# Optimization experiments

Measured on AMD Instinct MI355X. Metric: run time of the kernel, lower is better.

Reference implementation:

```python
import jax, jax.numpy as jnp
import numpy as np


def conv2d(x, w, b, pad):
    # NCHW / OIHW conv, stride 1
    y = jax.lax.conv_general_dilated(x, w, (1, 1), [(pad, pad), (pad, pad)],
                                     dimension_numbers=('NCHW', 'OIHW', 'NCHW'))
    return y + b[None, :, None, None]


def deform_conv2d(x, offset, modulator, w_reg, b_reg):
    # Faithful reimplementation of torchvision.ops.deform_conv2d (stride=1,
    # pad=K//2, dilation=1, 1 offset group), offset layout [B, 2*K*K, H, W]
    # with (dy, dx) pairs per kernel tap.
    B, C, H, W = x.shape
    K = w_reg.shape[-1]
    KK = K * K
    pad = K // 2
    off = offset.reshape(B, KK, 2, H, W)
    ks_y = (jnp.arange(KK) // K - pad).astype(x.dtype)
    ks_x = (jnp.arange(KK) % K - pad).astype(x.dtype)
    hh = jnp.arange(H, dtype=x.dtype)
    ww = jnp.arange(W, dtype=x.dtype)
    # sampling coords per (batch, kernel tap, out_y, out_x)
    py = hh[None, None, :, None] + ks_y[None, :, None, None] + off[:, :, 0]
    px = ww[None, None, None, :] + ks_x[None, :, None, None] + off[:, :, 1]
    y0 = jnp.floor(py)
    x0 = jnp.floor(px)
    ly = py - y0
    lx = px - x0
    y0i = y0.astype(jnp.int32)
    x0i = x0.astype(jnp.int32)
    x_flat = x.reshape(B, C, H * W)

    def gather(yi, xi, wgt):
        valid = (yi >= 0) & (yi < H) & (xi >= 0) & (xi < W)
        idx = (jnp.clip(yi, 0, H - 1) * W + jnp.clip(xi, 0, W - 1)).reshape(B, KK, H * W)
        v = jnp.take_along_axis(x_flat[:, :, None, :], idx[:, None], axis=3)  # [B,C,KK,HW]
        w = (wgt * valid.astype(x.dtype)).reshape(B, 1, KK, H * W)
        return v * w

    v = (gather(y0i, x0i, (1 - ly) * (1 - lx))
         + gather(y0i, x0i + 1, (1 - ly) * lx)
         + gather(y0i + 1, x0i, ly * (1 - lx))
         + gather(y0i + 1, x0i + 1, ly * lx))
    v = v * modulator.reshape(B, 1, KK, H * W)
    out = jnp.einsum('bckn,ock->bon', v, w_reg.reshape(w_reg.shape[0], C, KK))
    return out.reshape(B, -1, H, W) + b_reg[None, :, None, None]


def setup_inputs() -> dict:
    key = jax.random.key(0)
    ks = jax.random.split(key, 14)
    B, C, H, W = 8, 256, 64, 64
    K = 3
    Cr = C // 4  # SE ratio=4
    x = jax.random.normal(ks[0], (B, C, H, W), jnp.float32)
    # small offset-conv weights keep sampled offsets modest (torchvision inits these to 0)
    w_off = jax.random.normal(ks[1], (2 * K * K, C, K, K), jnp.float32) * 0.01
    b_off = jax.random.normal(ks[2], (2 * K * K,), jnp.float32) * 0.01
    w_mod = jax.random.normal(ks[3], (K * K, C, K, K), jnp.float32) * 0.01
    b_mod = jax.random.normal(ks[4], (K * K,), jnp.float32) * 0.01
    w_reg = jax.random.normal(ks[5], (C, C, K, K), jnp.float32) * (1.0 / np.sqrt(C * K * K))
    b_reg = jax.random.normal(ks[6], (C,), jnp.float32) * 0.01
    w_se1 = jax.random.normal(ks[7], (Cr, C), jnp.float32) * (1.0 / np.sqrt(C))
    b_se1 = jnp.zeros((Cr,), jnp.float32)
    w_se2 = jax.random.normal(ks[8], (C, Cr), jnp.float32) * (1.0 / np.sqrt(Cr))
    b_se2 = jnp.zeros((C,), jnp.float32)
    w_mask = jax.random.normal(ks[9], (C, C, 1, 1), jnp.float32) * (1.0 / np.sqrt(C))
    b_mask = jnp.zeros((C,), jnp.float32)
    return {"x": x, "w_off": w_off, "b_off": b_off, "w_mod": w_mod, "b_mod": b_mod,
            "w_reg": w_reg, "b_reg": b_reg, "w_se1": w_se1, "b_se1": b_se1,
            "w_se2": w_se2, "b_se2": b_se2, "w_mask": w_mask, "b_mask": b_mask}


def reference(x, w_off, b_off, w_mod, b_mod, w_reg, b_reg,
              w_se1, b_se1, w_se2, b_se2, w_mask, b_mask):
    # DeformableConv2d
    offset = conv2d(x, w_off, b_off, pad=1)
    modulator = 2.0 * jax.nn.sigmoid(conv2d(x, w_mod, b_mod, pad=1))
    f = deform_conv2d(x, offset, modulator, w_reg, b_reg)
    # SEBlock('avg', ch, ratio=4)
    s = jnp.mean(f, axis=(2, 3))                       # [B, C]
    s = jax.nn.relu(s @ w_se1.T + b_se1)               # [B, C/4]
    s = jax.nn.sigmoid(s @ w_se2.T + b_se2)            # [B, C]
    f = f * s[:, :, None, None]
    # mask = Hardsigmoid(Conv1x1(x))
    m = conv2d(x, w_mask, b_mask, pad=0)
    m = jnp.clip(m / 6.0 + 0.5, 0.0, 1.0)
    return f * m + x
```

## Files before the change

### kernel.cpp

```cpp
#include <hip/hip_runtime.h>
#include <math.h>

#define HWSZ 4096
#define C_ 256
#define B_ 8

#define M_WS      0
#define XB_WS     4194304
#define WT2_WS    8388608
#define SMEAN_WS  8753152
#define SSCALE_WS 8755200

typedef __attribute__((ext_vector_type(8))) short short8;
typedef __attribute__((ext_vector_type(4))) float f32x4;

__device__ __forceinline__ uint bfr(float a) {
  uint u = __float_as_uint(a);
  return (u + 0x7fffu + ((u >> 16) & 1u)) >> 16;
}
__device__ __forceinline__ uint pk2(float a, float b) { return bfr(a) | (bfr(b) << 16); }
__device__ __forceinline__ float bff(ushort u) { return __uint_as_float((uint)u << 16); }
__device__ __forceinline__ float lo16(uint u) { return __uint_as_float(u << 16); }
__device__ __forceinline__ float hi16(uint u) { return __uint_as_float(u & 0xffff0000u); }

__global__ __launch_bounds__(256) void k0_weights(
    const float* __restrict__ w_reg, const float* __restrict__ w_mask,
    const float* __restrict__ w_off, const float* __restrict__ w_mod,
    float* __restrict__ ws) {
  int i = blockIdx.x * 256 + threadIdx.x;
  const int nwt = 10 * 65536;
  const int total = nwt + 9 * 32 * 256;
  if (i >= total) {
    int z = i - total;
    if (z < 2048) ws[SMEAN_WS + z] = 0.f;
    return;
  }
  float v;
  if (i < 9 * 65536) {
    int kk = i >> 16, o = (i >> 8) & 255, c = i & 255;
    v = w_reg[(o * C_ + c) * 9 + kk];
  } else if (i < nwt) {
    v = w_mask[i - 9 * 65536];
  } else {
    int e = i - nwt;
    int s = e >> 13, r = e & 8191;
    int o2 = r >> 8, c = r & 255;
    if (o2 < 18)      v = w_off[(o2 * C_ + c) * 9 + s];
    else if (o2 < 27) v = w_mod[((o2 - 18) * C_ + c) * 9 + s];
    else              v = 0.f;
  }
  ((ushort*)(ws + WT2_WS))[i] = (ushort)bfr(v);
}

__global__ __launch_bounds__(256) void k0b_nhwc(const float* __restrict__ x,
                                                float* __restrict__ ws) {
  __shared__ float tile[64][65];
  int b = blockIdx.x >> 6, hw0 = (blockIdx.x & 63) << 6;
  int t = threadIdx.x;
  uint* xb = (uint*)(ws + XB_WS) + ((size_t)b << 19);
  int rr = t >> 6, cc = t & 63;
  int e = t & 7, hwp = t >> 3;
  for (int cg = 0; cg < 4; cg++) {
    __syncthreads();
    const float* xp = x + ((size_t)(b * 256 + cg * 64 + rr)) * HWSZ + hw0 + cc;
    #pragma unroll
    for (int r0 = 0; r0 < 64; r0 += 4)
      tile[r0 + rr][cc] = xp[(size_t)r0 * HWSZ];
    __syncthreads();
    #pragma unroll
    for (int h2 = 0; h2 < 2; h2++) {
      int hw_l = h2 * 32 + hwp;
      int c2 = e * 8;
      uint4 val;
      val.x = pk2(tile[c2][hw_l], tile[c2 + 1][hw_l]);
      val.y = pk2(tile[c2 + 2][hw_l], tile[c2 + 3][hw_l]);
      val.z = pk2(tile[c2 + 4][hw_l], tile[c2 + 5][hw_l]);
      val.w = pk2(tile[c2 + 6][hw_l], tile[c2 + 7][hw_l]);
      *(uint4*)&xb[(size_t)(hw0 + hw_l) * 128 + cg * 32 + e * 4] = val;
    }
  }
}

__global__ __launch_bounds__(512, 4) void k2_fused(
    const float* __restrict__ b_off, const float* __restrict__ b_mod,
    const float* __restrict__ b_reg, const float* __restrict__ b_mask,
    float* __restrict__ ws, float* __restrict__ out) {
  __shared__ uint vbraw[2][66 * 128];
  __shared__ float omrf[9 * 64 * 4];

  int bl = ((blockIdx.x & 7) << 6) | (blockIdx.x >> 3);
  int b = bl >> 6, h = bl & 63;
  int t = threadIdx.x;
  int lane = t & 63, w = t >> 6;
  const int hwid = t >> 5;
  const int cl = lane & 31;
  const ushort* xb2 = (const ushort*)(ws + XB_WS) + ((size_t)b << 20);
  const ushort* wt2 = (const ushort*)(ws + WT2_WS);
  const ushort* wom = wt2 + 10 * 65536;
  const int fr = lane & 15, fq = lane >> 4;

  auto widxP = [&](int pcol) -> uint {
    return (uint)pcol * 128u + (((uint)cl * 4u) ^ ((uint)(pcol & 7) << 2));
  };
  auto stageRow = [&](int row, int buf) {
    bool rv = ((unsigned)row < 64u);
    #pragma unroll
    for (int p = 0; p < 4; p++) {
      int pcol = p * 16 + hwid;
      int col = pcol - 1;
      uint4 v = make_uint4(0, 0, 0, 0);
      if (rv && ((unsigned)col < 64u))
        v = *(const uint4*)(xb2 + ((size_t)(row * 64 + col)) * 256 + cl * 8);
      *(uint4*)&vbraw[buf][widxP(pcol)] = v;
    }
    if (hwid < 2) {
      int pcol = 64 + hwid;
      int col = pcol - 1;
      uint4 v = make_uint4(0, 0, 0, 0);
      if (rv && col < 64)
        v = *(const uint4*)(xb2 + ((size_t)(row * 64 + col)) * 256 + cl * 8);
      *(uint4*)&vbraw[buf][widxP(pcol)] = v;
    }
  };
  auto makeRecs = [&](int kk, int nl, float* wg, int* ix) {
    const float4 rec = *(const float4*)&omrf[kk * 256 + nl * 4];
    float dy = rec.x, dx = rec.y, md = rec.z;
    float py = (float)(h + kk / 3 - 1) + dy;
    float px = (float)(nl + kk % 3 - 1) + dx;
    float fy = floorf(py), fx = floorf(px);
    float ly = py - fy, lx = px - fx;
    int y0 = (int)fy, x0 = (int)fx;
    int y1 = y0 + 1, x1 = x0 + 1;
    float vy0 = ((unsigned)y0 < 64u) ? 1.f : 0.f;
    float vy1 = ((unsigned)y1 < 64u) ? 1.f : 0.f;
    float vx0 = ((unsigned)x0 < 64u) ? 1.f : 0.f;
    float vx1 = ((unsigned)x1 < 64u) ? 1.f : 0.f;
    int cy0 = min(max(y0, 0), 63), cy1 = min(max(y1, 0), 63);
    int cx0 = min(max(x0, 0), 63), cx1 = min(max(x1, 0), 63);
    ix[0] = cy0 * 64 + cx0; wg[0] = (1.f - ly) * (1.f - lx) * md * vy0 * vx0;
    ix[1] = cy0 * 64 + cx1; wg[1] = (1.f - ly) * lx * md * vy0 * vx1;
    ix[2] = cy1 * 64 + cx0; wg[2] = ly * (1.f - lx) * md * vy1 * vx0;
    ix[3] = cy1 * 64 + cx1; wg[3] = ly * lx * md * vy1 * vx1;
  };
  auto gatherTap = [&](int kk, int buf) {
    #pragma unroll
    for (int p = 0; p < 4; p++) {
      int n = p * 16 + hwid;
      float wg[4]; int ix[4];
      makeRecs(kk, n, wg, ix);
      float a0 = 0.f, a1 = 0.f, a2 = 0.f, a3 = 0.f, a4 = 0.f, a5 = 0.f, a6 = 0.f, a7 = 0.f;
      #pragma unroll
      for (int cr = 0; cr < 4; cr++) {
        uint4 dd = *(const uint4*)(xb2 + (size_t)ix[cr] * 256 + cl * 8);
        float wv = wg[cr];
        a0 = fmaf(wv, lo16(dd.x), a0); a1 = fmaf(wv, hi16(dd.x), a1);
        a2 = fmaf(wv, lo16(dd.y), a2); a3 = fmaf(wv, hi16(dd.y), a3);
        a4 = fmaf(wv, lo16(dd.z), a4); a5 = fmaf(wv, hi16(dd.z), a5);
        a6 = fmaf(wv, lo16(dd.w), a6); a7 = fmaf(wv, hi16(dd.w), a7);
      }
      *(uint4*)&vbraw[buf][widxP(n)] =
          make_uint4(pk2(a0, a1), pk2(a2, a3), pk2(a4, a5), pk2(a6, a7));
    }
  };

  f32x4 aom = (f32x4)0.f;
  const int m0 = w >> 2, nt0 = w & 3;
  const int o0 = w << 5;
  f32x4 acc[2][4];
  #pragma unroll
  for (int mt = 0; mt < 2; mt++)
    #pragma unroll
    for (int nt = 0; nt < 4; nt++) acc[mt][nt] = (f32x4)0.f;
  ushort* mws = (ushort*)(ws + M_WS);
  float* sme = ws + SMEAN_WS + b * 256;

  stageRow(h - 1, 0);
  __syncthreads();
  for (int e = 0; e < 3; e++) {
    const int buf = (e == 1) ? 1 : 0;
    {
      const int bnA = nt0 * 16 + fr;
      #pragma unroll
      for (int s3 = 0; s3 < 3; s3++) {
        int s = e * 3 + s3;
        const ushort* wp = wom + (size_t)s * 8192;
        int pcol = bnA + s3;
        for (int ks = 0; ks < 8; ks++) {
          short8 af = *(const short8*)(wp + (m0 * 16 + fr) * 256 + ks * 32 + fq * 8);
          uint idx = (uint)pcol * 128u + (((uint)(ks * 16 + fq * 4)) ^ ((uint)(pcol & 7) << 2));
          short8 bf = *(const short8*)&vbraw[buf][idx];
          aom = __builtin_amdgcn_mfma_f32_16x16x32_bf16(af, bf, aom, 0, 0, 0);
        }
      }
    }
    if (e == 1) {
      const ushort* wt9 = wt2 + (size_t)9 * 65536;
      __builtin_amdgcn_s_setprio(1);
      for (int ks = 0; ks < 8; ks++) {
        short8 af0 = *(const short8*)(wt9 + (o0 + fr) * 256 + ks * 32 + fq * 8);
        short8 af1 = *(const short8*)(wt9 + (o0 + 16 + fr) * 256 + ks * 32 + fq * 8);
        #pragma unroll
        for (int nt = 0; nt < 4; nt++) {
          int pcol = nt * 16 + fr + 1;
          uint idx = (uint)pcol * 128u + (((uint)(ks * 16 + fq * 4)) ^ ((uint)(pcol & 7) << 2));
          short8 bf = *(const short8*)&vbraw[1][idx];
          acc[0][nt] = __builtin_amdgcn_mfma_f32_16x16x32_bf16(af0, bf, acc[0][nt], 0, 0, 0);
          acc[1][nt] = __builtin_amdgcn_mfma_f32_16x16x32_bf16(af1, bf, acc[1][nt], 0, 0, 0);
        }
      }
      __builtin_amdgcn_s_setprio(0);
    }
    if (e == 0)      stageRow(h, 1);
    else if (e == 1) stageRow(h + 1, 0);
    else {
      #pragma unroll
      for (int mt = 0; mt < 2; mt++)
        #pragma unroll
        for (int r = 0; r < 4; r++) {
          int o = o0 + mt * 16 + fq * 4 + r;
          float bm = b_mask[o];
          ushort* mp = mws + (size_t)(b * C_ + o) * HWSZ + h * 64;
          #pragma unroll
          for (int nt = 0; nt < 4; nt++) {
            float mv = fminf(fmaxf((acc[mt][nt][r] + bm) * (1.f / 6.f) + 0.5f, 0.f), 1.f);
            mp[nt * 16 + fr] = (ushort)bfr(mv);
            acc[mt][nt][r] = 0.f;
          }
        }
      #pragma unroll
      for (int r = 0; r < 4; r++) {
        int o = m0 * 16 + fq * 4 + r;
        int nn = nt0 * 16 + fr;
        if (o < 18) {
          omrf[(o >> 1) * 256 + nn * 4 + (o & 1)] = aom[r] + b_off[o];
        } else if (o < 27) {
          float v = aom[r] + b_mod[o - 18];
          omrf[(o - 18) * 256 + nn * 4 + 2] = 2.f / (1.f + expf(-v));
        }
      }
    }
    __syncthreads();
  }

  gatherTap(0, 1);
  __syncthreads();
  for (int kk = 0; kk < 9; kk++) {
    const int cur = (kk & 1) ^ 1;
    const ushort* wtap = wt2 + (size_t)kk * 65536;
    __builtin_amdgcn_s_setprio(1);
    for (int ks = 0; ks < 8; ks++) {
      short8 af0 = *(const short8*)(wtap + (o0 + fr) * 256 + ks * 32 + fq * 8);
      short8 af1 = *(const short8*)(wtap + (o0 + 16 + fr) * 256 + ks * 32 + fq * 8);
      #pragma unroll
      for (int nt = 0; nt < 4; nt++) {
        int bn = nt * 16 + fr;
        uint idx = (uint)bn * 128u + (((uint)(ks * 16 + fq * 4)) ^ ((uint)(bn & 7) << 2));
        short8 bf = *(const short8*)&vbraw[cur][idx];
        acc[0][nt] = __builtin_amdgcn_mfma_f32_16x16x32_bf16(af0, bf, acc[0][nt], 0, 0, 0);
        acc[1][nt] = __builtin_amdgcn_mfma_f32_16x16x32_bf16(af1, bf, acc[1][nt], 0, 0, 0);
      }
    }
    __builtin_amdgcn_s_setprio(0);
    if (kk < 8) {
      gatherTap(kk + 1, cur ^ 1);
      __syncthreads();
    }
  }

  #pragma unroll
  for (int mt = 0; mt < 2; mt++)
    #pragma unroll
    for (int r = 0; r < 4; r++) {
      int o = o0 + mt * 16 + fq * 4 + r;
      float bo = b_reg[o];
      float* op = out + (size_t)(b * C_ + o) * HWSZ + h * 64;
      float so = 0.f;
      #pragma unroll
      for (int nt = 0; nt < 4; nt++) {
        float fv = acc[mt][nt][r] + bo;
        op[nt * 16 + fr] = fv;
        so += fv;
      }
      so += __shfl_xor(so, 1);
      so += __shfl_xor(so, 2);
      so += __shfl_xor(so, 4);
      so += __shfl_xor(so, 8);
      if (fr == 0) atomicAdd(&sme[o], so);
    }
}

__global__ __launch_bounds__(256) void k4_se(
    const float* __restrict__ w_se1, const float* __restrict__ b_se1,
    const float* __restrict__ w_se2, const float* __restrict__ b_se2,
    float* __restrict__ ws) {
  __shared__ float sm[256];
  __shared__ float s1[64];
  int b = blockIdx.x;
  int t = threadIdx.x;
  sm[t] = ws[SMEAN_WS + b * 256 + t] * (1.f / HWSZ);
  __syncthreads();
  if (t < 64) {
    float a = b_se1[t];
    for (int c = 0; c < 256; c++) a += sm[c] * w_se1[t * 256 + c];
    s1[t] = fmaxf(a, 0.f);
  }
  __syncthreads();
  {
    float a = b_se2[t];
    for (int cr = 0; cr < 64; cr++) a += s1[cr] * w_se2[t * 64 + cr];
    ws[SSCALE_WS + b * 256 + t] = 1.f / (1.f + expf(-a));
  }
}

__global__ __launch_bounds__(256) void k5_final(const float* __restrict__ x,
                                                const float* __restrict__ ws,
                                                float* __restrict__ out) {
  const ushort* mws = (const ushort*)(ws + M_WS);
  int i4 = blockIdx.x * 256 + threadIdx.x;
  const int total = B_ * C_ * HWSZ / 4;
  for (; i4 < total; i4 += gridDim.x * 256) {
    int i = i4 * 4;
    int bc = i >> 12;
    float s = ws[SSCALE_WS + bc];
    float4 f = *(const float4*)&out[i];
    uint2 mu = *(const uint2*)&mws[i];
    float4 xv = *(const float4*)&x[i];
    float4 r;
    r.x = f.x * s * bff((ushort)(mu.x & 0xffffu)) + xv.x;
    r.y = f.y * s * bff((ushort)(mu.x >> 16)) + xv.y;
    r.z = f.z * s * bff((ushort)(mu.y & 0xffffu)) + xv.z;
    r.w = f.w * s * bff((ushort)(mu.y >> 16)) + xv.w;
    *(float4*)&out[i] = r;
  }
}

extern "C" void kernel_launch(void* const* d_in, const int* in_sizes, int n_in,
                              void* d_out, int out_size, void* d_ws, size_t ws_size,
                              hipStream_t stream) {
  const float* x      = (const float*)d_in[0];
  const float* w_off  = (const float*)d_in[1];
  const float* b_off  = (const float*)d_in[2];
  const float* w_mod  = (const float*)d_in[3];
  const float* b_mod  = (const float*)d_in[4];
  const float* w_reg  = (const float*)d_in[5];
  const float* b_reg  = (const float*)d_in[6];
  const float* w_se1  = (const float*)d_in[7];
  const float* b_se1  = (const float*)d_in[8];
  const float* w_se2  = (const float*)d_in[9];
  const float* b_se2  = (const float*)d_in[10];
  const float* w_mask = (const float*)d_in[11];
  const float* b_mask = (const float*)d_in[12];
  float* out = (float*)d_out;
  float* ws  = (float*)d_ws;

  k0_weights<<<dim3(2856), dim3(256), 0, stream>>>(w_reg, w_mask, w_off, w_mod, ws);
  k0b_nhwc<<<dim3(512), dim3(256), 0, stream>>>(x, ws);
  k2_fused<<<dim3(512), dim3(512), 0, stream>>>(b_off, b_mod, b_reg, b_mask, ws, out);
  k4_se<<<dim3(8), dim3(256), 0, stream>>>(w_se1, b_se1, w_se2, b_se2, ws);
  k5_final<<<dim3(2048), dim3(256), 0, stream>>>(x, ws, out);
}
```

Measured before the change: 194.8 us.

## Process two output rows per block to share staged input rows

The fused deformable-conv kernel now has 1024-thread blocks, each covering two adjacent output rows, with 256 blocks instead of 512. Each half of the block runs the offset/modulator and mask convolutions for its own row. The halves share the four staged input rows, where two single-row blocks staged six. The gather and tap GEMM loop then fill and consume a 128-column LDS buffer. This cuts redundant input staging and repeated weight fetches, but the larger LDS footprint allows only one block per CU and lengthens the per-block critical path.

```diff
diff --git a/kernel.cpp b/kernel.cpp
--- a/kernel.cpp
+++ b/kernel.cpp
@@ -81,51 +81,43 @@
   }
 }
 
-__global__ __launch_bounds__(512, 4) void k2_fused(
+__global__ __launch_bounds__(1024, 4) void k2_fused(
     const float* __restrict__ b_off, const float* __restrict__ b_mod,
     const float* __restrict__ b_reg, const float* __restrict__ b_mask,
     float* __restrict__ ws, float* __restrict__ out) {
-  __shared__ uint vbraw[2][66 * 128];
-  __shared__ float omrf[9 * 64 * 4];
-
-  int bl = ((blockIdx.x & 7) << 6) | (blockIdx.x >> 3);
-  int b = bl >> 6, h = bl & 63;
+  __shared__ uint vb[2][128 * 128];
+  __shared__ float omrf[2 * 9 * 64 * 4];
+
+  int bl = ((blockIdx.x & 7) << 5) | (blockIdx.x >> 3);
+  int b = bl >> 5, h0 = (bl & 31) << 1;
   int t = threadIdx.x;
   int lane = t & 63, w = t >> 6;
-  const int hwid = t >> 5;
+  const int hw = t >> 5;
   const int cl = lane & 31;
   const ushort* xb2 = (const ushort*)(ws + XB_WS) + ((size_t)b << 20);
   const ushort* wt2 = (const ushort*)(ws + WT2_WS);
   const ushort* wom = wt2 + 10 * 65536;
   const int fr = lane & 15, fq = lane >> 4;
-
-  auto widxP = [&](int pcol) -> uint {
-    return (uint)pcol * 128u + (((uint)cl * 4u) ^ ((uint)(pcol & 7) << 2));
+  const int rowhalf = w >> 3;
+  const int wv8 = w & 7;
+
+  auto widx = [&](int P) -> uint {
+    return (uint)P * 128u + (((uint)cl * 4u) ^ ((uint)(P & 7) << 2));
   };
   auto stageRow = [&](int row, int buf) {
     bool rv = ((unsigned)row < 64u);
-    #pragma unroll
-    for (int p = 0; p < 4; p++) {
-      int pcol = p * 16 + hwid;
-      int col = pcol - 1;
+    for (int pc = hw; pc < 66; pc += 32) {
+      int col = pc - 1;
       uint4 v = make_uint4(0, 0, 0, 0);
       if (rv && ((unsigned)col < 64u))
         v = *(const uint4*)(xb2 + ((size_t)(row * 64 + col)) * 256 + cl * 8);
-      *(uint4*)&vbraw[buf][widxP(pcol)] = v;
-    }
-    if (hwid < 2) {
-      int pcol = 64 + hwid;
-      int col = pcol - 1;
-      uint4 v = make_uint4(0, 0, 0, 0);
-      if (rv && col < 64)
-        v = *(const uint4*)(xb2 + ((size_t)(row * 64 + col)) * 256 + cl * 8);
-      *(uint4*)&vbraw[buf][widxP(pcol)] = v;
+      *(uint4*)&vb[buf][widx(pc)] = v;
     }
   };
-  auto makeRecs = [&](int kk, int nl, float* wg, int* ix) {
-    const float4 rec = *(const float4*)&omrf[kk * 256 + nl * 4];
+  auto makeRecs = [&](int rloc, int kk, int nl, float* wg, int* ix) {
+    const float4 rec = *(const float4*)&omrf[((rloc * 9 + kk) * 64 + nl) * 4];
     float dy = rec.x, dx = rec.y, md = rec.z;
-    float py = (float)(h + kk / 3 - 1) + dy;
+    float py = (float)(h0 + rloc + kk / 3 - 1) + dy;
     float px = (float)(nl + kk % 3 - 1) + dx;
     float fy = floorf(py), fx = floorf(px);
     float ly = py - fy, lx = px - fx;
@@ -145,9 +137,9 @@
   auto gatherTap = [&](int kk, int buf) {
     #pragma unroll
     for (int p = 0; p < 4; p++) {
-      int n = p * 16 + hwid;
+      int P = p * 32 + hw;
       float wg[4]; int ix[4];
-      makeRecs(kk, n, wg, ix);
+      makeRecs(P >> 6, kk, P & 63, wg, ix);
       float a0 = 0.f, a1 = 0.f, a2 = 0.f, a3 = 0.f, a4 = 0.f, a5 = 0.f, a6 = 0.f, a7 = 0.f;
       #pragma unroll
       for (int cr = 0; cr < 4; cr++) {
@@ -158,14 +150,15 @@
         a4 = fmaf(wv, lo16(dd.z), a4); a5 = fmaf(wv, hi16(dd.z), a5);
         a6 = fmaf(wv, lo16(dd.w), a6); a7 = fmaf(wv, hi16(dd.w), a7);
       }
-      *(uint4*)&vbraw[buf][widxP(n)] =
+      *(uint4*)&vb[buf][widx(P)] =
           make_uint4(pk2(a0, a1), pk2(a2, a3), pk2(a4, a5), pk2(a6, a7));
     }
   };
 
   f32x4 aom = (f32x4)0.f;
-  const int m0 = w >> 2, nt0 = w & 3;
-  const int o0 = w << 5;
+  const int m0 = wv8 >> 2, nt0 = wv8 & 3;
+  const int o0 = wv8 << 5;
+  const int hme = h0 + rowhalf;
   f32x4 acc[2][4];
   #pragma unroll
   for (int mt = 0; mt < 2; mt++)
@@ -174,26 +167,28 @@
   ushort* mws = (ushort*)(ws + M_WS);
   float* sme = ws + SMEAN_WS + b * 256;
 
-  stageRow(h - 1, 0);
-  __syncthreads();
-  for (int e = 0; e < 3; e++) {
-    const int buf = (e == 1) ? 1 : 0;
-    {
+  stageRow(h0 - 1, 0);
+  __syncthreads();
+  for (int e = 0; e < 4; e++) {
+    const int buf = e & 1;
+    const int g = (rowhalf == 0) ? e : e - 1;
+    if (g >= 0 && g < 3) {
       const int bnA = nt0 * 16 + fr;
       #pragma unroll
       for (int s3 = 0; s3 < 3; s3++) {
-        int s = e * 3 + s3;
+        int s = g * 3 + s3;
         const ushort* wp = wom + (size_t)s * 8192;
         int pcol = bnA + s3;
+        uint idxb = (uint)pcol * 128u;
+        uint xr = (uint)(pcol & 7) << 2;
         for (int ks = 0; ks < 8; ks++) {
           short8 af = *(const short8*)(wp + (m0 * 16 + fr) * 256 + ks * 32 + fq * 8);
-          uint idx = (uint)pcol * 128u + (((uint)(ks * 16 + fq * 4)) ^ ((uint)(pcol & 7) << 2));
-          short8 bf = *(const short8*)&vbraw[buf][idx];
+          short8 bf = *(const short8*)&vb[buf][idxb + (((uint)(ks * 16 + fq * 4)) ^ xr)];
           aom = __builtin_amdgcn_mfma_f32_16x16x32_bf16(af, bf, aom, 0, 0, 0);
         }
       }
     }
-    if (e == 1) {
+    if ((rowhalf == 0 && e == 1) || (rowhalf == 1 && e == 2)) {
       const ushort* wt9 = wt2 + (size_t)9 * 65536;
       __builtin_amdgcn_s_setprio(1);
       for (int ks = 0; ks < 8; ks++) {
@@ -203,23 +198,22 @@
         for (int nt = 0; nt < 4; nt++) {
           int pcol = nt * 16 + fr + 1;
           uint idx = (uint)pcol * 128u + (((uint)(ks * 16 + fq * 4)) ^ ((uint)(pcol & 7) << 2));
-          short8 bf = *(const short8*)&vbraw[1][idx];
+          short8 bf = *(const short8*)&vb[buf][idx];
           acc[0][nt] = __builtin_amdgcn_mfma_f32_16x16x32_bf16(af0, bf, acc[0][nt], 0, 0, 0);
           acc[1][nt] = __builtin_amdgcn_mfma_f32_16x16x32_bf16(af1, bf, acc[1][nt], 0, 0, 0);
         }
       }
       __builtin_amdgcn_s_setprio(0);
     }
-    if (e == 0)      stageRow(h, 1);
-    else if (e == 1) stageRow(h + 1, 0);
-    else {
+    if (e < 3) stageRow(h0 + e, (e + 1) & 1);
+    if (e == 3 && rowhalf == 0) {
       #pragma unroll
       for (int mt = 0; mt < 2; mt++)
         #pragma unroll
         for (int r = 0; r < 4; r++) {
           int o = o0 + mt * 16 + fq * 4 + r;
           float bm = b_mask[o];
-          ushort* mp = mws + (size_t)(b * C_ + o) * HWSZ + h * 64;
+          ushort* mp = mws + (size_t)(b * C_ + o) * HWSZ + hme * 64;
           #pragma unroll
           for (int nt = 0; nt < 4; nt++) {
             float mv = fminf(fmaxf((acc[mt][nt][r] + bm) * (1.f / 6.f) + 0.5f, 0.f), 1.f);
@@ -232,20 +226,49 @@
         int o = m0 * 16 + fq * 4 + r;
         int nn = nt0 * 16 + fr;
         if (o < 18) {
-          omrf[(o >> 1) * 256 + nn * 4 + (o & 1)] = aom[r] + b_off[o];
+          omrf[((0 * 9 + (o >> 1)) * 64 + nn) * 4 + (o & 1)] = aom[r] + b_off[o];
         } else if (o < 27) {
           float v = aom[r] + b_mod[o - 18];
-          omrf[(o - 18) * 256 + nn * 4 + 2] = 2.f / (1.f + expf(-v));
+          omrf[((0 * 9 + (o - 18)) * 64 + nn) * 4 + 2] = 2.f / (1.f + expf(-v));
         }
       }
     }
     __syncthreads();
   }
-
-  gatherTap(0, 1);
-  __syncthreads();
+  if (rowhalf == 1) {
+    #pragma unroll
+    for (int mt = 0; mt < 2; mt++)
+      #pragma unroll
+      for (int r = 0; r < 4; r++) {
+        int o = o0 + mt * 16 + fq * 4 + r;
+        float bm = b_mask[o];
+        ushort* mp = mws + (size_t)(b * C_ + o) * HWSZ + hme * 64;
+        #pragma unroll
+        for (int nt = 0; nt < 4; nt++) {
+          float mv = fminf(fmaxf((acc[mt][nt][r] + bm) * (1.f / 6.f) + 0.5f, 0.f), 1.f);
+          mp[nt * 16 + fr] = (ushort)bfr(mv);
+          acc[mt][nt][r] = 0.f;
+        }
+      }
+    #pragma unroll
+    for (int r = 0; r < 4; r++) {
+      int o = m0 * 16 + fq * 4 + r;
+      int nn = nt0 * 16 + fr;
+      if (o < 18) {
+        omrf[((1 * 9 + (o >> 1)) * 64 + nn) * 4 + (o & 1)] = aom[r] + b_off[o];
+      } else if (o < 27) {
+        float v = aom[r] + b_mod[o - 18];
+        omrf[((1 * 9 + (o - 18)) * 64 + nn) * 4 + 2] = 2.f / (1.f + expf(-v));
+      }
+    }
+  }
+  __syncthreads();
+
+  gatherTap(0, 0);
+  __syncthreads();
+  const int Pbase = rowhalf * 64;
   for (int kk = 0; kk < 9; kk++) {
-    const int cur = (kk & 1) ^ 1;
+    const int cur = kk & 1;
     const ushort* wtap = wt2 + (size_t)kk * 65536;
     __builtin_amdgcn_s_setprio(1);
     for (int ks = 0; ks < 8; ks++) {
@@ -253,9 +276,9 @@
       short8 af1 = *(const short8*)(wtap + (o0 + 16 + fr) * 256 + ks * 32 + fq * 8);
       #pragma unroll
       for (int nt = 0; nt < 4; nt++) {
-        int bn = nt * 16 + fr;
-        uint idx = (uint)bn * 128u + (((uint)(ks * 16 + fq * 4)) ^ ((uint)(bn & 7) << 2));
-        short8 bf = *(const short8*)&vbraw[cur][idx];
+        int P = Pbase + nt * 16 + fr;
+        uint idx = (uint)P * 128u + (((uint)(ks * 16 + fq * 4)) ^ ((uint)(P & 7) << 2));
+        short8 bf = *(const short8*)&vb[cur][idx];
         acc[0][nt] = __builtin_amdgcn_mfma_f32_16x16x32_bf16(af0, bf, acc[0][nt], 0, 0, 0);
         acc[1][nt] = __builtin_amdgcn_mfma_f32_16x16x32_bf16(af1, bf, acc[1][nt], 0, 0, 0);
       }
@@ -273,7 +296,7 @@
     for (int r = 0; r < 4; r++) {
       int o = o0 + mt * 16 + fq * 4 + r;
       float bo = b_reg[o];
-      float* op = out + (size_t)(b * C_ + o) * HWSZ + h * 64;
+      float* op = out + (size_t)(b * C_ + o) * HWSZ + hme * 64;
       float so = 0.f;
       #pragma unroll
       for (int nt = 0; nt < 4; nt++) {
@@ -355,7 +378,7 @@
 
   k0_weights<<<dim3(2856), dim3(256), 0, stream>>>(w_reg, w_mask, w_off, w_mod, ws);
   k0b_nhwc<<<dim3(512), dim3(256), 0, stream>>>(x, ws);
-  k2_fused<<<dim3(512), dim3(512), 0, stream>>>(b_off, b_mod, b_reg, b_mask, ws, out);
+  k2_fused<<<dim3(256), dim3(1024), 0, stream>>>(b_off, b_mod, b_reg, b_mask, ws, out);
   k4_se<<<dim3(8), dim3(256), 0, stream>>>(w_se1, b_se1, w_se2, b_se2, ws);
   k5_final<<<dim3(2048), dim3(256), 0, stream>>>(x, ws, out);
 }
```

New measurement: 243.9 us. 25.2% more time.

## Switch intermediate storage and MFMA from bf16 to fp16 with packed half2 bilinear gather

Applied to the files above, without the earlier changes.

Converts the weights, the NHWC copy of x, the mask buffer and the MFMA inputs from bf16 to fp16. This lets the deformable bilinear gather accumulate with packed __hfma2 on half2 pairs instead of unpacking to fp32 FMAs and repacking with manual rounding. The gather loop is also restructured to issue the loads for two positions ahead of the combine, so memory latency overlaps with arithmetic. Doing the gather accumulation in fp16 adds rounding error, and fp16 has less dynamic range than bf16 for large activations.

```diff
diff --git a/kernel.cpp b/kernel.cpp
--- a/kernel.cpp
+++ b/kernel.cpp
@@ -1,4 +1,5 @@
 #include <hip/hip_runtime.h>
+#include <hip/hip_fp16.h>
 #include <math.h>
 
 #define HWSZ 4096
@@ -14,14 +15,15 @@
 typedef __attribute__((ext_vector_type(8))) short short8;
 typedef __attribute__((ext_vector_type(4))) float f32x4;
 
-__device__ __forceinline__ uint bfr(float a) {
-  uint u = __float_as_uint(a);
-  return (u + 0x7fffu + ((u >> 16) & 1u)) >> 16;
-}
-__device__ __forceinline__ uint pk2(float a, float b) { return bfr(a) | (bfr(b) << 16); }
-__device__ __forceinline__ float bff(ushort u) { return __uint_as_float((uint)u << 16); }
-__device__ __forceinline__ float lo16(uint u) { return __uint_as_float(u << 16); }
-__device__ __forceinline__ float hi16(uint u) { return __uint_as_float(u & 0xffff0000u); }
+__device__ __forceinline__ ushort f2h(float a) {
+  __half h = __float2half(a);
+  return *reinterpret_cast<ushort*>(&h);
+}
+__device__ __forceinline__ uint hpk2(float a, float b) {
+  return (uint)f2h(a) | ((uint)f2h(b) << 16);
+}
+__device__ __forceinline__ uint h2u(__half2 h) { return *reinterpret_cast<uint*>(&h); }
+__device__ __forceinline__ __half2 u2h(uint u) { return *reinterpret_cast<__half2*>(&u); }
 
 __global__ __launch_bounds__(256) void k0_weights(
     const float* __restrict__ w_reg, const float* __restrict__ w_mask,
@@ -49,7 +51,7 @@
     else if (o2 < 27) v = w_mod[((o2 - 18) * C_ + c) * 9 + s];
     else              v = 0.f;
   }
-  ((ushort*)(ws + WT2_WS))[i] = (ushort)bfr(v);
+  ((ushort*)(ws + WT2_WS))[i] = f2h(v);
 }
 
 __global__ __launch_bounds__(256) void k0b_nhwc(const float* __restrict__ x,
@@ -72,10 +74,10 @@
       int hw_l = h2 * 32 + hwp;
       int c2 = e * 8;
       uint4 val;
-      val.x = pk2(tile[c2][hw_l], tile[c2 + 1][hw_l]);
-      val.y = pk2(tile[c2 + 2][hw_l], tile[c2 + 3][hw_l]);
-      val.z = pk2(tile[c2 + 4][hw_l], tile[c2 + 5][hw_l]);
-      val.w = pk2(tile[c2 + 6][hw_l], tile[c2 + 7][hw_l]);
+      val.x = hpk2(tile[c2][hw_l], tile[c2 + 1][hw_l]);
+      val.y = hpk2(tile[c2 + 2][hw_l], tile[c2 + 3][hw_l]);
+      val.z = hpk2(tile[c2 + 4][hw_l], tile[c2 + 5][hw_l]);
+      val.w = hpk2(tile[c2 + 6][hw_l], tile[c2 + 7][hw_l]);
       *(uint4*)&xb[(size_t)(hw0 + hw_l) * 128 + cg * 32 + e * 4] = val;
     }
   }
@@ -122,7 +124,7 @@
       *(uint4*)&vbraw[buf][widxP(pcol)] = v;
     }
   };
-  auto makeRecs = [&](int kk, int nl, float* wg, int* ix) {
+  auto loadPos = [&](int kk, int nl, uint4* d, float* wg) {
     const float4 rec = *(const float4*)&omrf[kk * 256 + nl * 4];
     float dy = rec.x, dx = rec.y, md = rec.z;
     float py = (float)(h + kk / 3 - 1) + dy;
@@ -137,30 +139,40 @@
     float vx1 = ((unsigned)x1 < 64u) ? 1.f : 0.f;
     int cy0 = min(max(y0, 0), 63), cy1 = min(max(y1, 0), 63);
     int cx0 = min(max(x0, 0), 63), cx1 = min(max(x1, 0), 63);
-    ix[0] = cy0 * 64 + cx0; wg[0] = (1.f - ly) * (1.f - lx) * md * vy0 * vx0;
-    ix[1] = cy0 * 64 + cx1; wg[1] = (1.f - ly) * lx * md * vy0 * vx1;
-    ix[2] = cy1 * 64 + cx0; wg[2] = ly * (1.f - lx) * md * vy1 * vx0;
-    ix[3] = cy1 * 64 + cx1; wg[3] = ly * lx * md * vy1 * vx1;
+    int ix0 = cy0 * 64 + cx0, ix1 = cy0 * 64 + cx1;
+    int ix2 = cy1 * 64 + cx0, ix3 = cy1 * 64 + cx1;
+    wg[0] = (1.f - ly) * (1.f - lx) * md * vy0 * vx0;
+    wg[1] = (1.f - ly) * lx * md * vy0 * vx1;
+    wg[2] = ly * (1.f - lx) * md * vy1 * vx0;
+    wg[3] = ly * lx * md * vy1 * vx1;
+    d[0] = *(const uint4*)(xb2 + (size_t)ix0 * 256 + cl * 8);
+    d[1] = *(const uint4*)(xb2 + (size_t)ix1 * 256 + cl * 8);
+    d[2] = *(const uint4*)(xb2 + (size_t)ix2 * 256 + cl * 8);
+    d[3] = *(const uint4*)(xb2 + (size_t)ix3 * 256 + cl * 8);
+  };
+  auto combineF16 = [&](const uint4* d, const float* wg) -> uint4 {
+    __half2 a0 = __float2half2_rn(0.f), a1 = a0, a2 = a0, a3 = a0;
+    #pragma unroll
+    for (int cr = 0; cr < 4; cr++) {
+      __half2 w2 = __float2half2_rn(wg[cr]);
+      a0 = __hfma2(w2, u2h(d[cr].x), a0);
+      a1 = __hfma2(w2, u2h(d[cr].y), a1);
+      a2 = __hfma2(w2, u2h(d[cr].z), a2);
+      a3 = __hfma2(w2, u2h(d[cr].w), a3);
+    }
+    return make_uint4(h2u(a0), h2u(a1), h2u(a2), h2u(a3));
   };
   auto gatherTap = [&](int kk, int buf) {
-    #pragma unroll
-    for (int p = 0; p < 4; p++) {
-      int n = p * 16 + hwid;
-      float wg[4]; int ix[4];
-      makeRecs(kk, n, wg, ix);
-      float a0 = 0.f, a1 = 0.f, a2 = 0.f, a3 = 0.f, a4 = 0.f, a5 = 0.f, a6 = 0.f, a7 = 0.f;
-      #pragma unroll
-      for (int cr = 0; cr < 4; cr++) {
-        uint4 dd = *(const uint4*)(xb2 + (size_t)ix[cr] * 256 + cl * 8);
-        float wv = wg[cr];
-        a0 = fmaf(wv, lo16(dd.x), a0); a1 = fmaf(wv, hi16(dd.x), a1);
-        a2 = fmaf(wv, lo16(dd.y), a2); a3 = fmaf(wv, hi16(dd.y), a3);
-        a4 = fmaf(wv, lo16(dd.z), a4); a5 = fmaf(wv, hi16(dd.z), a5);
-        a6 = fmaf(wv, lo16(dd.w), a6); a7 = fmaf(wv, hi16(dd.w), a7);
-      }
-      *(uint4*)&vbraw[buf][widxP(n)] =
-          make_uint4(pk2(a0, a1), pk2(a2, a3), pk2(a4, a5), pk2(a6, a7));
-    }
+    uint4 dA[4], dB[4];
+    float wgA[4], wgB[4];
+    loadPos(kk, 0 * 16 + hwid, dA, wgA);
+    loadPos(kk, 1 * 16 + hwid, dB, wgB);
+    *(uint4*)&vbraw[buf][widxP(0 * 16 + hwid)] = combineF16(dA, wgA);
+    loadPos(kk, 2 * 16 + hwid, dA, wgA);
+    *(uint4*)&vbraw[buf][widxP(1 * 16 + hwid)] = combineF16(dB, wgB);
+    loadPos(kk, 3 * 16 + hwid, dB, wgB);
+    *(uint4*)&vbraw[buf][widxP(2 * 16 + hwid)] = combineF16(dA, wgA);
+    *(uint4*)&vbraw[buf][widxP(3 * 16 + hwid)] = combineF16(dB, wgB);
   };
 
   f32x4 aom = (f32x4)0.f;
@@ -189,7 +201,7 @@
           short8 af = *(const short8*)(wp + (m0 * 16 + fr) * 256 + ks * 32 + fq * 8);
           uint idx = (uint)pcol * 128u + (((uint)(ks * 16 + fq * 4)) ^ ((uint)(pcol & 7) << 2));
           short8 bf = *(const short8*)&vbraw[buf][idx];
-          aom = __builtin_amdgcn_mfma_f32_16x16x32_bf16(af, bf, aom, 0, 0, 0);
+          aom = __builtin_amdgcn_mfma_f32_16x16x32_f16(af, bf, aom, 0, 0, 0);
         }
       }
     }
@@ -204,8 +216,8 @@
           int pcol = nt * 16 + fr + 1;
           uint idx = (uint)pcol * 128u + (((uint)(ks * 16 + fq * 4)) ^ ((uint)(pcol & 7) << 2));
           short8 bf = *(const short8*)&vbraw[1][idx];
-          acc[0][nt] = __builtin_amdgcn_mfma_f32_16x16x32_bf16(af0, bf, acc[0][nt], 0, 0, 0);
-          acc[1][nt] = __builtin_amdgcn_mfma_f32_16x16x32_bf16(af1, bf, acc[1][nt], 0, 0, 0);
+          acc[0][nt] = __builtin_amdgcn_mfma_f32_16x16x32_f16(af0, bf, acc[0][nt], 0, 0, 0);
+          acc[1][nt] = __builtin_amdgcn_mfma_f32_16x16x32_f16(af1, bf, acc[1][nt], 0, 0, 0);
         }
       }
       __builtin_amdgcn_s_setprio(0);
@@ -223,7 +235,7 @@
           #pragma unroll
           for (int nt = 0; nt < 4; nt++) {
             float mv = fminf(fmaxf((acc[mt][nt][r] + bm) * (1.f / 6.f) + 0.5f, 0.f), 1.f);
-            mp[nt * 16 + fr] = (ushort)bfr(mv);
+            mp[nt * 16 + fr] = f2h(mv);
             acc[mt][nt][r] = 0.f;
           }
         }
@@ -256,8 +268,8 @@
         int bn = nt * 16 + fr;
         uint idx = (uint)bn * 128u + (((uint)(ks * 16 + fq * 4)) ^ ((uint)(bn & 7) << 2));
         short8 bf = *(const short8*)&vbraw[cur][idx];
-        acc[0][nt] = __builtin_amdgcn_mfma_f32_16x16x32_bf16(af0, bf, acc[0][nt], 0, 0, 0);
-        acc[1][nt] = __builtin_amdgcn_mfma_f32_16x16x32_bf16(af1, bf, acc[1][nt], 0, 0, 0);
+        acc[0][nt] = __builtin_amdgcn_mfma_f32_16x16x32_f16(af0, bf, acc[0][nt], 0, 0, 0);
+        acc[1][nt] = __builtin_amdgcn_mfma_f32_16x16x32_f16(af1, bf, acc[1][nt], 0, 0, 0);
       }
     }
     __builtin_amdgcn_s_setprio(0);
@@ -325,11 +337,13 @@
     float4 f = *(const float4*)&out[i];
     uint2 mu = *(const uint2*)&mws[i];
     float4 xv = *(const float4*)&x[i];
+    float2 ma = __half22float2(u2h(mu.x));
+    float2 mb = __half22float2(u2h(mu.y));
     float4 r;
-    r.x = f.x * s * bff((ushort)(mu.x & 0xffffu)) + xv.x;
-    r.y = f.y * s * bff((ushort)(mu.x >> 16)) + xv.y;
-    r.z = f.z * s * bff((ushort)(mu.y & 0xffffu)) + xv.z;
-    r.w = f.w * s * bff((ushort)(mu.y >> 16)) + xv.w;
+    r.x = f.x * s * ma.x + xv.x;
+    r.y = f.y * s * ma.y + xv.y;
+    r.z = f.z * s * mb.x + xv.z;
+    r.w = f.w * s * mb.y + xv.w;
     *(float4*)&out[i] = r;
   }
 }
```

Measured after the change: 182.9 us. 1.06x faster.
